# Kernel optimization log

Hardware: AMD Instinct MI355X
Metric: run time of the kernel (lower is better)

Reference implementation:

```python
import jax, jax.numpy as jnp
import numpy as np

N_NODES = 50000


def spmm(rows, cols, vals, dense):
    # out[i,:] = sum_{e: rows[e]==i} vals[e] * dense[cols[e], :]
    gathered = dense[cols] * vals[:, None]  # [E, D]
    return jax.ops.segment_sum(gathered, rows, num_segments=N_NODES)


def setup_inputs() -> dict:
    key = jax.random.key(0)
    k1, k2, k3, k4, k5, k6 = jax.random.split(key, 6)
    N, E, F, H, C = N_NODES, 800000, 512, 256, 64
    node_features = jax.random.normal(k1, (N, F), dtype=jnp.float32)
    adj_rows = jax.random.randint(k2, (E,), 0, N, dtype=jnp.int32)
    adj_cols = jax.random.randint(k3, (E,), 0, N, dtype=jnp.int32)
    adj_vals = jax.random.uniform(k4, (E,), dtype=jnp.float32)
    W1 = jax.random.normal(k5, (F, H), dtype=jnp.float32) * (1.0 / np.sqrt(F))
    b1 = jnp.zeros((H,), dtype=jnp.float32)
    W2 = jax.random.normal(k6, (H, C), dtype=jnp.float32) * (1.0 / np.sqrt(H))
    b2 = jnp.zeros((C,), dtype=jnp.float32)
    return {"node_features": node_features, "adj_rows": adj_rows,
            "adj_cols": adj_cols, "adj_vals": adj_vals,
            "W1": W1, "b1": b1, "W2": W2, "b2": b2}


def reference(node_features, adj_rows, adj_cols, adj_vals, W1, b1, W2, b2):
    # Layer 1: dense projection then sparse aggregation, then ReLU.
    support1 = node_features @ W1 + b1           # [N, H]
    x = jax.nn.relu(spmm(adj_rows, adj_cols, adj_vals, support1))
    # Dropout is identity in eval mode (training=False).
    # Layer 2
    support2 = x @ W2 + b2                       # [N, C]
    x = spmm(adj_rows, adj_cols, adj_vals, support2)
    return jax.nn.log_softmax(x, axis=1)
```

## Files before the change

### kernel.cpp

```cpp
#include <hip/hip_runtime.h>

#define N_NODES 50000
#define N_EDGES 800000
#define F_IN    512
#define H_DIM   256
#define C_DIM   64
#define MPAD    50048

#define NB      196
#define NCHUNK  49
#define CHUNK   16384
#define BCAP    6144

typedef __bf16 bf16;
typedef __bf16 bf16x4 __attribute__((ext_vector_type(4)));
typedef __bf16 bf16x8 __attribute__((ext_vector_type(8)));
typedef float  f32x4  __attribute__((ext_vector_type(4)));
typedef unsigned int u32;
typedef unsigned long long u64;
typedef unsigned char u8;

__device__ __forceinline__ void gl_lds16(const void* g, void* l) {
    __builtin_amdgcn_global_load_lds(
        (const __attribute__((address_space(1))) u32*)g,
        (__attribute__((address_space(3))) u32*)l, 16, 0, 0);
}

__device__ __forceinline__ float unpack_val(u32 pk) {
    return __builtin_bit_cast(float, pk << 16);
}


__global__ __launch_bounds__(1024) void prep_k(const int* __restrict__ rows,
                                               const float* __restrict__ W1,
                                               const float* __restrict__ W2,
                                               u32* __restrict__ G,
                                               bf16* __restrict__ W1t,
                                               bf16* __restrict__ W2t) {
    __shared__ u32 h[16 * NB];
    int bid = blockIdx.x, tid = threadIdx.x;
    if (bid < NCHUNK) {
        int wid = tid >> 6;
        for (int i = tid; i < 16 * NB; i += 1024) h[i] = 0;
        __syncthreads();
        int base = bid * CHUNK;
        int end = base + CHUNK; if (end > N_EDGES) end = N_EDGES;
        for (int e = base + tid; e < end; e += 1024)
            atomicAdd(&h[wid * NB + (rows[e] >> 8)], 1);
        __syncthreads();
        if (tid < NB) {
            u32 s = 0;
#pragma unroll
            for (int w = 0; w < 16; w++) s += h[w * NB + tid];
            G[tid * NCHUNK + bid] = s;
        }
    } else {
        int i = (bid - NCHUNK) * 1024 + tid;
        if (i < F_IN * H_DIM) {
            int k = i >> 8, n = i & 255;
            W1t[n * F_IN + k] = (bf16)W1[i];
        } else {
            int j = i - F_IN * H_DIM;
            if (j < H_DIM * C_DIM) {
                int k = j >> 6, n = j & 63;
                W2t[n * H_DIM + k] = (bf16)W2[j];
            }
        }
    }
}


__global__ __launch_bounds__(1024) void scatterB_k(const int* __restrict__ rows,
                                                   const int* __restrict__ cols,
                                                   const float* __restrict__ vals,
                                                   const u32* __restrict__ G,
                                                   u32* __restrict__ epack,
                                                   u8* __restrict__ lrow) {
    __shared__ u32 cur[NB];
    __shared__ u32 wtot[16];
    int tid = threadIdx.x, wid = tid >> 6, lane = tid & 63;
    int c = blockIdx.x;
    u32 tot = 0, pre = 0;
    if (tid < NB) {
        for (int cc = 0; cc < NCHUNK; cc++) {
            u32 v = G[tid * NCHUNK + cc];
            tot += v;
            if (cc < c) pre += v;
        }
    }
    u32 incl = tot;
#pragma unroll
    for (int off = 1; off < 64; off <<= 1) {
        u32 u = __shfl_up(incl, off, 64);
        if (lane >= off) incl += u;
    }
    if (lane == 63) wtot[wid] = incl;
    __syncthreads();
    u32 wpre = 0;
#pragma unroll
    for (int w = 0; w < 16; w++)
        if (w < wid) wpre += wtot[w];
    if (tid < NB) cur[tid] = (wpre + incl - tot) + pre;
    __syncthreads();
    int base = c * CHUNK;
    int end = base + CHUNK; if (end > N_EDGES) end = N_EDGES;
    for (int e = base + tid; e < end; e += 1024) {
        int r = rows[e];
        unsigned short vb = __builtin_bit_cast(unsigned short, (bf16)vals[e]);
        u32 pk = ((u32)cols[e] << 16) | (u32)vb;
        u32 p = atomicAdd(&cur[r >> 8], 1);
        epack[p] = pk;
        lrow[p] = (u8)(r & 255);
    }
}


__global__ __launch_bounds__(256) void sortC_k(u32* __restrict__ epack,
                                               const u8* __restrict__ lrow,
                                               const u32* __restrict__ G,
                                               int* __restrict__ starts) {
    __shared__ u32 edat[BCAP];
    __shared__ u32 sdat[BCAP];
    __shared__ u8  erow[BCAP];
    __shared__ u32 h[4 * 256];
    __shared__ u32 cur[256];
    __shared__ u32 wt1[4], wt2[4];
    __shared__ u32 sh_s, sh_n;
    int b = blockIdx.x, tid = threadIdx.x, wid = tid >> 6, lane = tid & 63;

    u32 btot = 0;
    if (tid < NB)
        for (int cc = 0; cc < NCHUNK; cc++) btot += G[tid * NCHUNK + cc];
    u32 bincl = btot;
#pragma unroll
    for (int off = 1; off < 64; off <<= 1) {
        u32 u = __shfl_up(bincl, off, 64);
        if (lane >= off) bincl += u;
    }
    if (lane == 63) wt1[wid] = bincl;
    __syncthreads();
    u32 bwpre = 0;
#pragma unroll
    for (int w = 0; w < 4; w++)
        if (w < wid) bwpre += wt1[w];
    if (tid == b) { sh_s = bwpre + bincl - btot; sh_n = btot; }
    __syncthreads();
    int s = (int)sh_s;
    int n = (int)sh_n;
    if (n > BCAP) n = BCAP;

    for (int i = tid; i < n; i += 256) { edat[i] = epack[s + i]; erow[i] = lrow[s + i]; }
    for (int i = tid; i < 1024; i += 256) h[i] = 0;
    __syncthreads();
    for (int i = tid; i < n; i += 256) atomicAdd(&h[wid * 256 + erow[i]], 1);
    __syncthreads();
    u32 tot = h[tid] + h[256 + tid] + h[512 + tid] + h[768 + tid];
    u32 incl = tot;
#pragma unroll
    for (int off = 1; off < 64; off <<= 1) {
        u32 u = __shfl_up(incl, off, 64);
        if (lane >= off) incl += u;
    }
    if (lane == 63) wt2[wid] = incl;
    __syncthreads();
    u32 wpre = 0;
#pragma unroll
    for (int w = 0; w < 4; w++)
        if (w < wid) wpre += wt2[w];
    u32 excl = wpre + incl - tot;
    cur[tid] = excl;
    int grow = b * 256 + tid;
    if (grow < N_NODES) starts[grow] = s + (int)excl;
    if (b == 0 && tid == 0) starts[N_NODES] = N_EDGES;
    __syncthreads();
    for (int i = tid; i < n; i += 256) {
        u32 p = atomicAdd(&cur[erow[i]], 1);
        sdat[p] = edat[i];
    }
    __syncthreads();
    for (int i = tid; i < n; i += 256) epack[s + i] = sdat[i];
}


__global__ __launch_bounds__(512) void gemm1_k(const float* __restrict__ A,
                                               const bf16* __restrict__ Bt,
                                               const float* __restrict__ bias,
                                               bf16* __restrict__ C) {
    constexpr int BM = 128, BK = 64;
    __shared__ bf16 As[BM * BK];
    __shared__ bf16 Bs[256 * BK];

    int tid = threadIdx.x;
    int wid = tid >> 6, lane = tid & 63;
    int wr = wid >> 2, wc = wid & 3;
    int l15 = lane & 15, hi = lane >> 4;
    int sw = l15 & 7;
    int bm = blockIdx.x;

    f32x4 acc[4][4];
#pragma unroll
    for (int m = 0; m < 4; m++)
#pragma unroll
        for (int n = 0; n < 4; n++) acc[m][n] = (f32x4){0.f, 0.f, 0.f, 0.f};

    for (int kt = 0; kt < F_IN; kt += BK) {
#pragma unroll
        for (int j = 0; j < 4; j++) {
            int ch = j * 512 + tid;
            int row = ch >> 3, kc = ch & 7;
            int kcs = kc ^ (row & 7);
            gl_lds16(Bt + (size_t)row * F_IN + kt + kcs * 8,
                     &Bs[(j * 512 + wid * 64) * 8]);
        }
#pragma unroll
        for (int j = 0; j < 2; j++) {
            int ch = j * 512 + tid;
            int row = ch >> 3, kc = ch & 7;
            int ar = bm * BM + row;
            if (ar >= N_NODES) ar = N_NODES - 1;
            const f32x4* src = (const f32x4*)(A + (size_t)ar * F_IN + kt + kc * 8);
            f32x4 u = src[0], v = src[1];
            bf16x8 o;
            o[0] = (bf16)u[0]; o[1] = (bf16)u[1]; o[2] = (bf16)u[2]; o[3] = (bf16)u[3];
            o[4] = (bf16)v[0]; o[5] = (bf16)v[1]; o[6] = (bf16)v[2]; o[7] = (bf16)v[3];
            *(bf16x8*)&As[row * BK + (kc ^ (row & 7)) * 8] = o;
        }
        __syncthreads();

        bf16x8 afr[2][4], bfr[2][4];
#pragma unroll
        for (int kk = 0; kk < 2; kk++) {
            int c = (kk * 4 + hi) ^ sw;
#pragma unroll
            for (int m = 0; m < 4; m++)
                afr[kk][m] = *(const bf16x8*)&As[(wr * 64 + m * 16 + l15) * BK + c * 8];
#pragma unroll
            for (int n = 0; n < 4; n++)
                bfr[kk][n] = *(const bf16x8*)&Bs[(wc * 64 + n * 16 + l15) * BK + c * 8];
        }
#pragma unroll
        for (int kk = 0; kk < 2; kk++)
#pragma unroll
            for (int m = 0; m < 4; m++)
#pragma unroll
                for (int n = 0; n < 4; n++)
                    acc[m][n] = __builtin_amdgcn_mfma_f32_16x16x32_bf16(
                        afr[kk][m], bfr[kk][n], acc[m][n], 0, 0, 0);
        __syncthreads();
    }

#pragma unroll
    for (int m = 0; m < 4; m++) {
        int row0 = bm * BM + wr * 64 + m * 16 + hi * 4;
#pragma unroll
        for (int n = 0; n < 4; n++) {
            int col = wc * 64 + n * 16 + l15;
            float bz = bias[col];
#pragma unroll
            for (int r = 0; r < 4; r++) {
                int row = row0 + r;
                if (row < N_NODES)
                    C[(size_t)row * H_DIM + col] = (bf16)(acc[m][n][r] + bz);
            }
        }
    }
}


__global__ __launch_bounds__(256) void gemm2_k(const bf16* __restrict__ A,
                                               const bf16* __restrict__ Bt,
                                               const float* __restrict__ bias,
                                               bf16* __restrict__ C) {
    constexpr int BM = 128, BK = 64;
    __shared__ bf16 As[BM * BK];
    __shared__ bf16 Bs[64 * BK];

    int tid = threadIdx.x;
    int wid = tid >> 6, lane = tid & 63;
    int wr = wid >> 1, wc = wid & 1;
    int l15 = lane & 15, hi = lane >> 4;
    int sw = l15 & 7;
    int bm = blockIdx.x;

    f32x4 acc[4][2];
#pragma unroll
    for (int m = 0; m < 4; m++)
#pragma unroll
        for (int n = 0; n < 2; n++) acc[m][n] = (f32x4){0.f, 0.f, 0.f, 0.f};

    for (int kt = 0; kt < H_DIM; kt += BK) {
#pragma unroll
        for (int j = 0; j < 4; j++) {
            int ch = j * 256 + tid;
            int row = ch >> 3, kc = ch & 7;
            int kcs = kc ^ (row & 7);
            gl_lds16(A + (size_t)(bm * BM + row) * H_DIM + kt + kcs * 8,
                     &As[(j * 256 + wid * 64) * 8]);
        }
#pragma unroll
        for (int j = 0; j < 2; j++) {
            int ch = j * 256 + tid;
            int row = ch >> 3, kc = ch & 7;
            int kcs = kc ^ (row & 7);
            gl_lds16(Bt + (size_t)row * H_DIM + kt + kcs * 8,
                     &Bs[(j * 256 + wid * 64) * 8]);
        }
        __syncthreads();

        bf16x8 afr[2][4], bfr[2][2];
#pragma unroll
        for (int kk = 0; kk < 2; kk++) {
            int c = (kk * 4 + hi) ^ sw;
#pragma unroll
            for (int m = 0; m < 4; m++)
                afr[kk][m] = *(const bf16x8*)&As[(wr * 64 + m * 16 + l15) * BK + c * 8];
#pragma unroll
            for (int n = 0; n < 2; n++)
                bfr[kk][n] = *(const bf16x8*)&Bs[(wc * 32 + n * 16 + l15) * BK + c * 8];
        }
#pragma unroll
        for (int kk = 0; kk < 2; kk++)
#pragma unroll
            for (int m = 0; m < 4; m++)
#pragma unroll
                for (int n = 0; n < 2; n++)
                    acc[m][n] = __builtin_amdgcn_mfma_f32_16x16x32_bf16(
                        afr[kk][m], bfr[kk][n], acc[m][n], 0, 0, 0);
        __syncthreads();
    }

#pragma unroll
    for (int m = 0; m < 4; m++) {
        int row0 = bm * BM + wr * 64 + m * 16 + hi * 4;
#pragma unroll
        for (int n = 0; n < 2; n++) {
            int col = wc * 32 + n * 16 + l15;
            float bz = bias[col];
#pragma unroll
            for (int r = 0; r < 4; r++) {
                int row = row0 + r;
                if (row < N_NODES)
                    C[(size_t)row * C_DIM + col] = (bf16)(acc[m][n][r] + bz);
            }
        }
    }
}


__global__ __launch_bounds__(256) void spmm1_k(const int* __restrict__ starts,
                                               const u32* __restrict__ epack,
                                               const bf16* __restrict__ s1,
                                               bf16* __restrict__ x16) {
    int wid = threadIdx.x >> 6, lane = threadIdx.x & 63;
    int row = blockIdx.x * 4 + wid;
    if (row >= N_NODES) return;
    int s = starts[row], e = starts[row + 1];
    f32x4 acc = (f32x4){0.f, 0.f, 0.f, 0.f};
    const bf16* s1l = s1 + lane * 4;
    int p = s;
    for (; p + 8 <= e; p += 8) {
        u32 k0 = __builtin_nontemporal_load(epack + p);
        u32 k1 = __builtin_nontemporal_load(epack + p + 1);
        u32 k2 = __builtin_nontemporal_load(epack + p + 2);
        u32 k3 = __builtin_nontemporal_load(epack + p + 3);
        u32 k4 = __builtin_nontemporal_load(epack + p + 4);
        u32 k5 = __builtin_nontemporal_load(epack + p + 5);
        u32 k6 = __builtin_nontemporal_load(epack + p + 6);
        u32 k7 = __builtin_nontemporal_load(epack + p + 7);
        bf16x4 g0 = *(const bf16x4*)(s1l + (size_t)(k0 >> 16) * H_DIM);
        bf16x4 g1 = *(const bf16x4*)(s1l + (size_t)(k1 >> 16) * H_DIM);
        bf16x4 g2 = *(const bf16x4*)(s1l + (size_t)(k2 >> 16) * H_DIM);
        bf16x4 g3 = *(const bf16x4*)(s1l + (size_t)(k3 >> 16) * H_DIM);
        bf16x4 g4 = *(const bf16x4*)(s1l + (size_t)(k4 >> 16) * H_DIM);
        bf16x4 g5 = *(const bf16x4*)(s1l + (size_t)(k5 >> 16) * H_DIM);
        bf16x4 g6 = *(const bf16x4*)(s1l + (size_t)(k6 >> 16) * H_DIM);
        bf16x4 g7 = *(const bf16x4*)(s1l + (size_t)(k7 >> 16) * H_DIM);
        float v0 = unpack_val(k0), v1 = unpack_val(k1), v2 = unpack_val(k2), v3 = unpack_val(k3);
        float v4 = unpack_val(k4), v5 = unpack_val(k5), v6 = unpack_val(k6), v7 = unpack_val(k7);
#pragma unroll
        for (int j = 0; j < 4; j++)
            acc[j] += v0 * (float)g0[j] + v1 * (float)g1[j] +
                      v2 * (float)g2[j] + v3 * (float)g3[j] +
                      v4 * (float)g4[j] + v5 * (float)g5[j] +
                      v6 * (float)g6[j] + v7 * (float)g7[j];
    }
    for (; p < e; ++p) {
        u32 k = __builtin_nontemporal_load(epack + p);
        float v = unpack_val(k);
        bf16x4 g = *(const bf16x4*)(s1l + (size_t)(k >> 16) * H_DIM);
#pragma unroll
        for (int j = 0; j < 4; j++) acc[j] += v * (float)g[j];
    }
    bf16x4 o;
#pragma unroll
    for (int j = 0; j < 4; j++) o[j] = (bf16)fmaxf(acc[j], 0.f);
    u64 bits = __builtin_bit_cast(u64, o);
    __builtin_nontemporal_store(bits, (u64*)(x16 + (size_t)row * H_DIM + lane * 4));
}


__global__ __launch_bounds__(256) void spmm2_sm_k(const int* __restrict__ starts,
                                                  const u32* __restrict__ epack,
                                                  const bf16* __restrict__ s2,
                                                  float* __restrict__ out) {
    int wid = threadIdx.x >> 6, lane = threadIdx.x & 63;
    int row = blockIdx.x * 4 + wid;
    if (row >= N_NODES) return;
    int s = starts[row], e = starts[row + 1];
    float acc = 0.f;
    int p = s;
    for (; p + 8 <= e; p += 8) {
        u32 k0 = __builtin_nontemporal_load(epack + p);
        u32 k1 = __builtin_nontemporal_load(epack + p + 1);
        u32 k2 = __builtin_nontemporal_load(epack + p + 2);
        u32 k3 = __builtin_nontemporal_load(epack + p + 3);
        u32 k4 = __builtin_nontemporal_load(epack + p + 4);
        u32 k5 = __builtin_nontemporal_load(epack + p + 5);
        u32 k6 = __builtin_nontemporal_load(epack + p + 6);
        u32 k7 = __builtin_nontemporal_load(epack + p + 7);
        float g0 = (float)s2[(size_t)(k0 >> 16) * C_DIM + lane];
        float g1 = (float)s2[(size_t)(k1 >> 16) * C_DIM + lane];
        float g2 = (float)s2[(size_t)(k2 >> 16) * C_DIM + lane];
        float g3 = (float)s2[(size_t)(k3 >> 16) * C_DIM + lane];
        float g4 = (float)s2[(size_t)(k4 >> 16) * C_DIM + lane];
        float g5 = (float)s2[(size_t)(k5 >> 16) * C_DIM + lane];
        float g6 = (float)s2[(size_t)(k6 >> 16) * C_DIM + lane];
        float g7 = (float)s2[(size_t)(k7 >> 16) * C_DIM + lane];
        acc += unpack_val(k0) * g0 + unpack_val(k1) * g1 +
               unpack_val(k2) * g2 + unpack_val(k3) * g3 +
               unpack_val(k4) * g4 + unpack_val(k5) * g5 +
               unpack_val(k6) * g6 + unpack_val(k7) * g7;
    }
    for (; p < e; ++p) {
        u32 k = __builtin_nontemporal_load(epack + p);
        acc += unpack_val(k) * (float)s2[(size_t)(k >> 16) * C_DIM + lane];
    }
    float mx = acc;
#pragma unroll
    for (int off = 32; off >= 1; off >>= 1) mx = fmaxf(mx, __shfl_xor(mx, off, 64));
    float ex = expf(acc - mx);
    float se = ex;
#pragma unroll
    for (int off = 32; off >= 1; off >>= 1) se += __shfl_xor(se, off, 64);
    __builtin_nontemporal_store((acc - mx) - logf(se),
                                out + (size_t)row * C_DIM + lane);
}


extern "C" void kernel_launch(void* const* d_in, const int* in_sizes, int n_in,
                              void* d_out, int out_size, void* d_ws, size_t ws_size,
                              hipStream_t stream) {
    const float* nf   = (const float*)d_in[0];
    const int*   rows = (const int*)d_in[1];
    const int*   cols = (const int*)d_in[2];
    const float* vals = (const float*)d_in[3];
    const float* W1   = (const float*)d_in[4];
    const float* b1   = (const float*)d_in[5];
    const float* W2   = (const float*)d_in[6];
    const float* b2   = (const float*)d_in[7];
    float* out = (float*)d_out;

    char* w = (char*)d_ws;
    auto alloc = [&](size_t b) { void* p = (void*)w; w += (b + 255) & ~(size_t)255; return p; };

    bf16* x16  = (bf16*)alloc((size_t)MPAD * H_DIM * 2);
    bf16* sup1 = (bf16*)alloc((size_t)N_NODES * H_DIM * 2);
    bf16* sup2 = sup1;
    bf16* W1t = (bf16*)alloc((size_t)H_DIM * F_IN * 2);
    bf16* W2t = (bf16*)alloc((size_t)C_DIM * H_DIM * 2);
    int* starts = (int*)alloc((size_t)(N_NODES + 1) * 4);
    u32* G      = (u32*)alloc((size_t)NB * NCHUNK * 4);
    u32* epack  = (u32*)alloc((size_t)N_EDGES * 4);
    u8*  lrow   = (u8*)alloc((size_t)N_EDGES);

    prep_k<<<NCHUNK + 144, 1024, 0, stream>>>(rows, W1, W2, G, W1t, W2t);
    scatterB_k<<<NCHUNK, 1024, 0, stream>>>(rows, cols, vals, G, epack, lrow);
    sortC_k<<<NB, 256, 0, stream>>>(epack, lrow, G, starts);
    gemm1_k<<<MPAD / 128, 512, 0, stream>>>(nf, W1t, b1, sup1);
    spmm1_k<<<(N_NODES + 3) / 4, 256, 0, stream>>>(starts, epack, sup1, x16);
    gemm2_k<<<MPAD / 128, 256, 0, stream>>>(x16, W2t, b2, sup2);
    spmm2_sm_k<<<(N_NODES + 3) / 4, 256, 0, stream>>>(starts, epack, sup2, out);

    (void)in_sizes; (void)n_in; (void)out_size; (void)ws_size;
}
```

Before: 191.6 us.

## Split SpMM1 feature dimension into slices with edge-parallel lane groups

Rewrites the first sparse aggregation so each block handles a 32-column slice of one row's features. Within a wave, four lane groups process different edges in parallel, each lane gathering bf16 pairs, and the partial sums are combined with cross-lane shuffles. The goal is more parallelism per row and more gathers in flight, since the previous kernel walked edges serially with full-row 8-byte gathers. In exchange the edge index stream is read eight times, gathers shrink to 4 bytes, and the grid becomes eight times larger.

```diff
diff --git a/kernel.cpp b/kernel.cpp
--- a/kernel.cpp
+++ b/kernel.cpp
@@ -13,6 +13,7 @@
 #define BCAP    6144
 
 typedef __bf16 bf16;
+typedef __bf16 bf16x2 __attribute__((ext_vector_type(2)));
 typedef __bf16 bf16x4 __attribute__((ext_vector_type(4)));
 typedef __bf16 bf16x8 __attribute__((ext_vector_type(8)));
 typedef float  f32x4  __attribute__((ext_vector_type(4)));
@@ -347,55 +348,46 @@
 }
 
 
-__global__ __launch_bounds__(256) void spmm1_k(const int* __restrict__ starts,
-                                               const u32* __restrict__ epack,
-                                               const bf16* __restrict__ s1,
-                                               bf16* __restrict__ x16) {
-    int wid = threadIdx.x >> 6, lane = threadIdx.x & 63;
-    int row = blockIdx.x * 4 + wid;
+__global__ __launch_bounds__(256) void spmm1x_k(const int* __restrict__ starts,
+                                                const u32* __restrict__ epack,
+                                                const bf16* __restrict__ s1,
+                                                bf16* __restrict__ x16) {
+    int tid = threadIdx.x, wid = tid >> 6, lane = tid & 63;
+    int g = lane >> 4, d2 = lane & 15;
+    int bid = blockIdx.x;
+    int sl = bid & 7, rb = bid >> 3;
+    int row = rb * 4 + wid;
     if (row >= N_NODES) return;
+    int dimoff = sl * 32 + d2 * 2;
+    const bf16* s1d = s1 + dimoff;
     int s = starts[row], e = starts[row + 1];
-    f32x4 acc = (f32x4){0.f, 0.f, 0.f, 0.f};
-    const bf16* s1l = s1 + lane * 4;
-    int p = s;
-    for (; p + 8 <= e; p += 8) {
-        u32 k0 = __builtin_nontemporal_load(epack + p);
-        u32 k1 = __builtin_nontemporal_load(epack + p + 1);
-        u32 k2 = __builtin_nontemporal_load(epack + p + 2);
-        u32 k3 = __builtin_nontemporal_load(epack + p + 3);
-        u32 k4 = __builtin_nontemporal_load(epack + p + 4);
-        u32 k5 = __builtin_nontemporal_load(epack + p + 5);
-        u32 k6 = __builtin_nontemporal_load(epack + p + 6);
-        u32 k7 = __builtin_nontemporal_load(epack + p + 7);
-        bf16x4 g0 = *(const bf16x4*)(s1l + (size_t)(k0 >> 16) * H_DIM);
-        bf16x4 g1 = *(const bf16x4*)(s1l + (size_t)(k1 >> 16) * H_DIM);
-        bf16x4 g2 = *(const bf16x4*)(s1l + (size_t)(k2 >> 16) * H_DIM);
-        bf16x4 g3 = *(const bf16x4*)(s1l + (size_t)(k3 >> 16) * H_DIM);
-        bf16x4 g4 = *(const bf16x4*)(s1l + (size_t)(k4 >> 16) * H_DIM);
-        bf16x4 g5 = *(const bf16x4*)(s1l + (size_t)(k5 >> 16) * H_DIM);
-        bf16x4 g6 = *(const bf16x4*)(s1l + (size_t)(k6 >> 16) * H_DIM);
-        bf16x4 g7 = *(const bf16x4*)(s1l + (size_t)(k7 >> 16) * H_DIM);
-        float v0 = unpack_val(k0), v1 = unpack_val(k1), v2 = unpack_val(k2), v3 = unpack_val(k3);
-        float v4 = unpack_val(k4), v5 = unpack_val(k5), v6 = unpack_val(k6), v7 = unpack_val(k7);
-#pragma unroll
-        for (int j = 0; j < 4; j++)
-            acc[j] += v0 * (float)g0[j] + v1 * (float)g1[j] +
-                      v2 * (float)g2[j] + v3 * (float)g3[j] +
-                      v4 * (float)g4[j] + v5 * (float)g5[j] +
-                      v6 * (float)g6[j] + v7 * (float)g7[j];
-    }
-    for (; p < e; ++p) {
-        u32 k = __builtin_nontemporal_load(epack + p);
-        float v = unpack_val(k);
-        bf16x4 g = *(const bf16x4*)(s1l + (size_t)(k >> 16) * H_DIM);
-#pragma unroll
-        for (int j = 0; j < 4; j++) acc[j] += v * (float)g[j];
-    }
-    bf16x4 o;
-#pragma unroll
-    for (int j = 0; j < 4; j++) o[j] = (bf16)fmaxf(acc[j], 0.f);
-    u64 bits = __builtin_bit_cast(u64, o);
-    __builtin_nontemporal_store(bits, (u64*)(x16 + (size_t)row * H_DIM + lane * 4));
+    float a0 = 0.f, a1 = 0.f;
+    for (int p = s; p < e; p += 16) {
+        int p0 = p + g, p1 = p + 4 + g, p2 = p + 8 + g, p3 = p + 12 + g;
+        u32 k0 = (p0 < e) ? __builtin_nontemporal_load(epack + p0) : 0u;
+        u32 k1 = (p1 < e) ? __builtin_nontemporal_load(epack + p1) : 0u;
+        u32 k2 = (p2 < e) ? __builtin_nontemporal_load(epack + p2) : 0u;
+        u32 k3 = (p3 < e) ? __builtin_nontemporal_load(epack + p3) : 0u;
+        bf16x2 g0 = *(const bf16x2*)(s1d + (size_t)(k0 >> 16) * H_DIM);
+        bf16x2 g1 = *(const bf16x2*)(s1d + (size_t)(k1 >> 16) * H_DIM);
+        bf16x2 g2 = *(const bf16x2*)(s1d + (size_t)(k2 >> 16) * H_DIM);
+        bf16x2 g3 = *(const bf16x2*)(s1d + (size_t)(k3 >> 16) * H_DIM);
+        float v0 = unpack_val(k0), v1 = unpack_val(k1);
+        float v2 = unpack_val(k2), v3 = unpack_val(k3);
+        a0 += v0 * (float)g0[0] + v1 * (float)g1[0] +
+              v2 * (float)g2[0] + v3 * (float)g3[0];
+        a1 += v0 * (float)g0[1] + v1 * (float)g1[1] +
+              v2 * (float)g2[1] + v3 * (float)g3[1];
+    }
+    a0 += __shfl_xor(a0, 16, 64); a0 += __shfl_xor(a0, 32, 64);
+    a1 += __shfl_xor(a1, 16, 64); a1 += __shfl_xor(a1, 32, 64);
+    if (g == 0) {
+        bf16x2 o;
+        o[0] = (bf16)fmaxf(a0, 0.f);
+        o[1] = (bf16)fmaxf(a1, 0.f);
+        u32 bits = __builtin_bit_cast(u32, o);
+        __builtin_nontemporal_store(bits, (u32*)(x16 + (size_t)row * H_DIM + dimoff));
+    }
 }
 
 
@@ -477,7 +469,7 @@
     scatterB_k<<<NCHUNK, 1024, 0, stream>>>(rows, cols, vals, G, epack, lrow);
     sortC_k<<<NB, 256, 0, stream>>>(epack, lrow, G, starts);
     gemm1_k<<<MPAD / 128, 512, 0, stream>>>(nf, W1t, b1, sup1);
-    spmm1_k<<<(N_NODES + 3) / 4, 256, 0, stream>>>(starts, epack, sup1, x16);
+    spmm1x_k<<<8 * ((N_NODES + 3) / 4), 256, 0, stream>>>(starts, epack, sup1, x16);
     gemm2_k<<<MPAD / 128, 256, 0, stream>>>(x16, W2t, b2, sup2);
     spmm2_sm_k<<<(N_NODES + 3) / 4, 256, 0, stream>>>(starts, epack, sup2, out);
 
```

New measurement: 267.6 us. 39.6% more time.

## Scatter edges chunk-locally and gather bucket segments in sort kernel

Applied to the files above, without the earlier changes.

The scatter kernel now writes each edge chunk's bucket-grouped output into a chunk-local region, so it only needs a per-chunk scan of 196 counts instead of a full global prefix over all chunks. The sort kernel then assembles each bucket from 49 chunk segments, using a binary search over segment offsets, and writes the final epack. This removes the serial 49-element G loops in the scatter kernel and keeps its scattered writes within a local 64KB window. In exchange it adds an extra intermediate buffer and per-element binary-search indexing in the sort kernel's load loop.

```diff
diff --git a/kernel.cpp b/kernel.cpp
--- a/kernel.cpp
+++ b/kernel.cpp
@@ -74,33 +74,31 @@
                                                    const int* __restrict__ cols,
                                                    const float* __restrict__ vals,
                                                    const u32* __restrict__ G,
-                                                   u32* __restrict__ epack,
-                                                   u8* __restrict__ lrow) {
+                                                   u32* __restrict__ epack_t,
+                                                   u8* __restrict__ lrow_t) {
     __shared__ u32 cur[NB];
-    __shared__ u32 wtot[16];
+    __shared__ u32 wt[4];
     int tid = threadIdx.x, wid = tid >> 6, lane = tid & 63;
     int c = blockIdx.x;
-    u32 tot = 0, pre = 0;
-    if (tid < NB) {
-        for (int cc = 0; cc < NCHUNK; cc++) {
-            u32 v = G[tid * NCHUNK + cc];
-            tot += v;
-            if (cc < c) pre += v;
-        }
-    }
-    u32 incl = tot;
-#pragma unroll
-    for (int off = 1; off < 64; off <<= 1) {
-        u32 u = __shfl_up(incl, off, 64);
-        if (lane >= off) incl += u;
-    }
-    if (lane == 63) wtot[wid] = incl;
-    __syncthreads();
-    u32 wpre = 0;
-#pragma unroll
-    for (int w = 0; w < 16; w++)
-        if (w < wid) wpre += wtot[w];
-    if (tid < NB) cur[tid] = (wpre + incl - tot) + pre;
+    u32 v = 0, incl = 0;
+    if (tid < 256) {
+        if (tid < NB) v = G[tid * NCHUNK + c];
+        incl = v;
+#pragma unroll
+        for (int off = 1; off < 64; off <<= 1) {
+            u32 u = __shfl_up(incl, off, 64);
+            if (lane >= off) incl += u;
+        }
+        if (lane == 63) wt[wid] = incl;
+    }
+    __syncthreads();
+    if (tid < 256) {
+        u32 wpre = 0;
+#pragma unroll
+        for (int w = 0; w < 4; w++)
+            if (w < wid) wpre += wt[w];
+        if (tid < NB) cur[tid] = wpre + incl - v;
+    }
     __syncthreads();
     int base = c * CHUNK;
     int end = base + CHUNK; if (end > N_EDGES) end = N_EDGES;
@@ -109,47 +107,60 @@
         unsigned short vb = __builtin_bit_cast(unsigned short, (bf16)vals[e]);
         u32 pk = ((u32)cols[e] << 16) | (u32)vb;
         u32 p = atomicAdd(&cur[r >> 8], 1);
-        epack[p] = pk;
-        lrow[p] = (u8)(r & 255);
-    }
-}
-
-
-__global__ __launch_bounds__(256) void sortC_k(u32* __restrict__ epack,
-                                               const u8* __restrict__ lrow,
+        epack_t[base + p] = pk;
+        lrow_t[base + p] = (u8)(r & 255);
+    }
+}
+
+
+__global__ __launch_bounds__(256) void sortC_k(const u32* __restrict__ epack_t,
+                                               const u8* __restrict__ lrow_t,
                                                const u32* __restrict__ G,
+                                               u32* __restrict__ epack,
                                                int* __restrict__ starts) {
     __shared__ u32 edat[BCAP];
     __shared__ u32 sdat[BCAP];
     __shared__ u8  erow[BCAP];
     __shared__ u32 h[4 * 256];
     __shared__ u32 cur[256];
-    __shared__ u32 wt1[4], wt2[4];
-    __shared__ u32 sh_s, sh_n;
+    __shared__ u32 wt2[4];
+    __shared__ u32 segoff[NCHUNK + 1];
+    __shared__ u32 segsrc[NCHUNK];
+    __shared__ u32 sh_s;
     int b = blockIdx.x, tid = threadIdx.x, wid = tid >> 6, lane = tid & 63;
 
-    u32 btot = 0;
-    if (tid < NB)
-        for (int cc = 0; cc < NCHUNK; cc++) btot += G[tid * NCHUNK + cc];
-    u32 bincl = btot;
-#pragma unroll
-    for (int off = 1; off < 64; off <<= 1) {
-        u32 u = __shfl_up(bincl, off, 64);
-        if (lane >= off) bincl += u;
-    }
-    if (lane == 63) wt1[wid] = bincl;
-    __syncthreads();
-    u32 bwpre = 0;
-#pragma unroll
-    for (int w = 0; w < 4; w++)
-        if (w < wid) bwpre += wt1[w];
-    if (tid == b) { sh_s = bwpre + bincl - btot; sh_n = btot; }
+    if (tid < 64) {
+        u32 len = 0, pre = 0;
+        if (tid < NCHUNK) {
+            for (int bb = 0; bb < b; bb++) pre += G[bb * NCHUNK + tid];
+            len = G[b * NCHUNK + tid];
+            segsrc[tid] = tid * CHUNK + pre;
+        }
+        u32 incl = len;
+#pragma unroll
+        for (int off = 1; off < 64; off <<= 1) {
+            u32 u = __shfl_up(incl, off, 64);
+            if (lane >= off) incl += u;
+        }
+        if (tid < NCHUNK) segoff[tid] = incl - len;
+        if (tid == 63) segoff[NCHUNK] = incl;
+        u32 ssum = pre;
+#pragma unroll
+        for (int off = 1; off < 64; off <<= 1) ssum += __shfl_xor(ssum, off, 64);
+        if (tid == 0) sh_s = ssum;
+    }
     __syncthreads();
     int s = (int)sh_s;
-    int n = (int)sh_n;
+    int n = (int)segoff[NCHUNK];
     if (n > BCAP) n = BCAP;
 
-    for (int i = tid; i < n; i += 256) { edat[i] = epack[s + i]; erow[i] = lrow[s + i]; }
+    for (int i = tid; i < n; i += 256) {
+        int lo = 0, hi = NCHUNK;
+        while (hi - lo > 1) { int mid = (lo + hi) >> 1; if ((int)segoff[mid] <= i) lo = mid; else hi = mid; }
+        u32 src = segsrc[lo] + (u32)(i - (int)segoff[lo]);
+        edat[i] = epack_t[src];
+        erow[i] = lrow_t[src];
+    }
     for (int i = tid; i < 1024; i += 256) h[i] = 0;
     __syncthreads();
     for (int i = tid; i < n; i += 256) atomicAdd(&h[wid * 256 + erow[i]], 1);
@@ -469,13 +480,14 @@
     bf16* W1t = (bf16*)alloc((size_t)H_DIM * F_IN * 2);
     bf16* W2t = (bf16*)alloc((size_t)C_DIM * H_DIM * 2);
     int* starts = (int*)alloc((size_t)(N_NODES + 1) * 4);
-    u32* G      = (u32*)alloc((size_t)NB * NCHUNK * 4);
-    u32* epack  = (u32*)alloc((size_t)N_EDGES * 4);
-    u8*  lrow   = (u8*)alloc((size_t)N_EDGES);
+    u32* G       = (u32*)alloc((size_t)NB * NCHUNK * 4);
+    u32* epack   = (u32*)alloc((size_t)N_EDGES * 4);
+    u32* epack_t = (u32*)alloc((size_t)NCHUNK * CHUNK * 4);
+    u8*  lrow_t  = (u8*)alloc((size_t)NCHUNK * CHUNK);
 
     prep_k<<<NCHUNK + 144, 1024, 0, stream>>>(rows, W1, W2, G, W1t, W2t);
-    scatterB_k<<<NCHUNK, 1024, 0, stream>>>(rows, cols, vals, G, epack, lrow);
-    sortC_k<<<NB, 256, 0, stream>>>(epack, lrow, G, starts);
+    scatterB_k<<<NCHUNK, 1024, 0, stream>>>(rows, cols, vals, G, epack_t, lrow_t);
+    sortC_k<<<NB, 256, 0, stream>>>(epack_t, lrow_t, G, epack, starts);
     gemm1_k<<<MPAD / 128, 512, 0, stream>>>(nf, W1t, b1, sup1);
     spmm1_k<<<(N_NODES + 3) / 4, 256, 0, stream>>>(starts, epack, sup1, x16);
     gemm2_k<<<MPAD / 128, 256, 0, stream>>>(x16, W2t, b2, sup2);
```

After: 207.3 us. 1.08x slower.

## Merge edge scatter and first GEMM into one heterogeneous launch

Applied to the files above, without the earlier changes.

Combines the edge bucketing scatter kernel and the layer-1 dense GEMM into a single kernel whose first blocks do the scatter and whose remaining blocks do GEMM tiles. The two are independent, so they can run concurrently on the GPU, filling the idle compute units left by the 49-block scatter and saving one launch. The scatter part now uses 512 threads instead of 1024, so each scatter block does more serial work. Shared memory is a union buffer sized for the GEMM.

```diff
diff --git a/kernel.cpp b/kernel.cpp
--- a/kernel.cpp
+++ b/kernel.cpp
@@ -70,47 +70,137 @@
 }
 
 
-__global__ __launch_bounds__(1024) void scatterB_k(const int* __restrict__ rows,
-                                                   const int* __restrict__ cols,
-                                                   const float* __restrict__ vals,
-                                                   const u32* __restrict__ G,
-                                                   u32* __restrict__ epack,
-                                                   u8* __restrict__ lrow) {
-    __shared__ u32 cur[NB];
-    __shared__ u32 wtot[16];
-    int tid = threadIdx.x, wid = tid >> 6, lane = tid & 63;
-    int c = blockIdx.x;
-    u32 tot = 0, pre = 0;
-    if (tid < NB) {
-        for (int cc = 0; cc < NCHUNK; cc++) {
-            u32 v = G[tid * NCHUNK + cc];
-            tot += v;
-            if (cc < c) pre += v;
-        }
-    }
-    u32 incl = tot;
-#pragma unroll
-    for (int off = 1; off < 64; off <<= 1) {
-        u32 u = __shfl_up(incl, off, 64);
-        if (lane >= off) incl += u;
-    }
-    if (lane == 63) wtot[wid] = incl;
-    __syncthreads();
-    u32 wpre = 0;
-#pragma unroll
-    for (int w = 0; w < 16; w++)
-        if (w < wid) wpre += wtot[w];
-    if (tid < NB) cur[tid] = (wpre + incl - tot) + pre;
-    __syncthreads();
-    int base = c * CHUNK;
-    int end = base + CHUNK; if (end > N_EDGES) end = N_EDGES;
-    for (int e = base + tid; e < end; e += 1024) {
-        int r = rows[e];
-        unsigned short vb = __builtin_bit_cast(unsigned short, (bf16)vals[e]);
-        u32 pk = ((u32)cols[e] << 16) | (u32)vb;
-        u32 p = atomicAdd(&cur[r >> 8], 1);
-        epack[p] = pk;
-        lrow[p] = (u8)(r & 255);
+__global__ __launch_bounds__(512) void sg_k(const int* __restrict__ rows,
+                                            const int* __restrict__ cols,
+                                            const float* __restrict__ vals,
+                                            const u32* __restrict__ G,
+                                            u32* __restrict__ epack,
+                                            u8* __restrict__ lrow,
+                                            const float* __restrict__ A,
+                                            const bf16* __restrict__ Bt,
+                                            const float* __restrict__ bias,
+                                            bf16* __restrict__ C) {
+    __shared__ __attribute__((aligned(16))) char smem[49152];
+    int bid = blockIdx.x, tid = threadIdx.x;
+    int wid = tid >> 6, lane = tid & 63;
+
+    if (bid < NCHUNK) {
+        u32* cur = (u32*)smem;
+        u32* wt  = (u32*)(smem + 1024);
+        int c = bid;
+        u32 tot = 0, pre = 0, incl = 0;
+        if (tid < 256) {
+            if (tid < NB) {
+                for (int cc = 0; cc < NCHUNK; cc++) {
+                    u32 v = G[tid * NCHUNK + cc];
+                    tot += v;
+                    if (cc < c) pre += v;
+                }
+            }
+            incl = tot;
+#pragma unroll
+            for (int off = 1; off < 64; off <<= 1) {
+                u32 u = __shfl_up(incl, off, 64);
+                if (lane >= off) incl += u;
+            }
+            if (lane == 63) wt[wid] = incl;
+        }
+        __syncthreads();
+        if (tid < 256) {
+            u32 wpre = 0;
+#pragma unroll
+            for (int w = 0; w < 4; w++)
+                if (w < wid) wpre += wt[w];
+            if (tid < NB) cur[tid] = (wpre + incl - tot) + pre;
+        }
+        __syncthreads();
+        int base = c * CHUNK;
+        int end = base + CHUNK; if (end > N_EDGES) end = N_EDGES;
+        for (int e = base + tid; e < end; e += 512) {
+            int r = rows[e];
+            unsigned short vb = __builtin_bit_cast(unsigned short, (bf16)vals[e]);
+            u32 pk = ((u32)cols[e] << 16) | (u32)vb;
+            u32 p = atomicAdd(&cur[r >> 8], 1);
+            epack[p] = pk;
+            lrow[p] = (u8)(r & 255);
+        }
+        return;
+    }
+
+    constexpr int BM = 128, BK = 64;
+    bf16* As = (bf16*)smem;
+    bf16* Bs = (bf16*)(smem + 16384);
+    int wr = wid >> 2, wc = wid & 3;
+    int l15 = lane & 15, hi = lane >> 4;
+    int sw = l15 & 7;
+    int bm = bid - NCHUNK;
+
+    f32x4 acc[4][4];
+#pragma unroll
+    for (int m = 0; m < 4; m++)
+#pragma unroll
+        for (int n = 0; n < 4; n++) acc[m][n] = (f32x4){0.f, 0.f, 0.f, 0.f};
+
+    for (int kt = 0; kt < F_IN; kt += BK) {
+#pragma unroll
+        for (int j = 0; j < 4; j++) {
+            int ch = j * 512 + tid;
+            int row = ch >> 3, kc = ch & 7;
+            int kcs = kc ^ (row & 7);
+            gl_lds16(Bt + (size_t)row * F_IN + kt + kcs * 8,
+                     &Bs[(j * 512 + wid * 64) * 8]);
+        }
+#pragma unroll
+        for (int j = 0; j < 2; j++) {
+            int ch = j * 512 + tid;
+            int row = ch >> 3, kc = ch & 7;
+            int ar = bm * BM + row;
+            if (ar >= N_NODES) ar = N_NODES - 1;
+            const f32x4* src = (const f32x4*)(A + (size_t)ar * F_IN + kt + kc * 8);
+            f32x4 u = src[0], v = src[1];
+            bf16x8 o;
+            o[0] = (bf16)u[0]; o[1] = (bf16)u[1]; o[2] = (bf16)u[2]; o[3] = (bf16)u[3];
+            o[4] = (bf16)v[0]; o[5] = (bf16)v[1]; o[6] = (bf16)v[2]; o[7] = (bf16)v[3];
+            *(bf16x8*)&As[row * BK + (kc ^ (row & 7)) * 8] = o;
+        }
+        __syncthreads();
+
+        bf16x8 afr[2][4], bfr[2][4];
+#pragma unroll
+        for (int kk = 0; kk < 2; kk++) {
+            int c = (kk * 4 + hi) ^ sw;
+#pragma unroll
+            for (int m = 0; m < 4; m++)
+                afr[kk][m] = *(const bf16x8*)&As[(wr * 64 + m * 16 + l15) * BK + c * 8];
+#pragma unroll
+            for (int n = 0; n < 4; n++)
+                bfr[kk][n] = *(const bf16x8*)&Bs[(wc * 64 + n * 16 + l15) * BK + c * 8];
+        }
+#pragma unroll
+        for (int kk = 0; kk < 2; kk++)
+#pragma unroll
+            for (int m = 0; m < 4; m++)
+#pragma unroll
+                for (int n = 0; n < 4; n++)
+                    acc[m][n] = __builtin_amdgcn_mfma_f32_16x16x32_bf16(
+                        afr[kk][m], bfr[kk][n], acc[m][n], 0, 0, 0);
+        __syncthreads();
+    }
+
+#pragma unroll
+    for (int m = 0; m < 4; m++) {
+        int row0 = bm * BM + wr * 64 + m * 16 + hi * 4;
+#pragma unroll
+        for (int n = 0; n < 4; n++) {
+            int col = wc * 64 + n * 16 + l15;
+            float bz = bias[col];
+#pragma unroll
+            for (int r = 0; r < 4; r++) {
+                int row = row0 + r;
+                if (row < N_NODES)
+                    C[(size_t)row * H_DIM + col] = (bf16)(acc[m][n][r] + bz);
+            }
+        }
     }
 }
 
@@ -179,91 +269,6 @@
     }
     __syncthreads();
     for (int i = tid; i < n; i += 256) epack[s + i] = sdat[i];
-}
-
-
-__global__ __launch_bounds__(512) void gemm1_k(const float* __restrict__ A,
-                                               const bf16* __restrict__ Bt,
-                                               const float* __restrict__ bias,
-                                               bf16* __restrict__ C) {
-    constexpr int BM = 128, BK = 64;
-    __shared__ bf16 As[BM * BK];
-    __shared__ bf16 Bs[256 * BK];
-
-    int tid = threadIdx.x;
-    int wid = tid >> 6, lane = tid & 63;
-    int wr = wid >> 2, wc = wid & 3;
-    int l15 = lane & 15, hi = lane >> 4;
-    int sw = l15 & 7;
-    int bm = blockIdx.x;
-
-    f32x4 acc[4][4];
-#pragma unroll
-    for (int m = 0; m < 4; m++)
-#pragma unroll
-        for (int n = 0; n < 4; n++) acc[m][n] = (f32x4){0.f, 0.f, 0.f, 0.f};
-
-    for (int kt = 0; kt < F_IN; kt += BK) {
-#pragma unroll
-        for (int j = 0; j < 4; j++) {
-            int ch = j * 512 + tid;
-            int row = ch >> 3, kc = ch & 7;
-            int kcs = kc ^ (row & 7);
-            gl_lds16(Bt + (size_t)row * F_IN + kt + kcs * 8,
-                     &Bs[(j * 512 + wid * 64) * 8]);
-        }
-#pragma unroll
-        for (int j = 0; j < 2; j++) {
-            int ch = j * 512 + tid;
-            int row = ch >> 3, kc = ch & 7;
-            int ar = bm * BM + row;
-            if (ar >= N_NODES) ar = N_NODES - 1;
-            const f32x4* src = (const f32x4*)(A + (size_t)ar * F_IN + kt + kc * 8);
-            f32x4 u = src[0], v = src[1];
-            bf16x8 o;
-            o[0] = (bf16)u[0]; o[1] = (bf16)u[1]; o[2] = (bf16)u[2]; o[3] = (bf16)u[3];
-            o[4] = (bf16)v[0]; o[5] = (bf16)v[1]; o[6] = (bf16)v[2]; o[7] = (bf16)v[3];
-            *(bf16x8*)&As[row * BK + (kc ^ (row & 7)) * 8] = o;
-        }
-        __syncthreads();
-
-        bf16x8 afr[2][4], bfr[2][4];
-#pragma unroll
-        for (int kk = 0; kk < 2; kk++) {
-            int c = (kk * 4 + hi) ^ sw;
-#pragma unroll
-            for (int m = 0; m < 4; m++)
-                afr[kk][m] = *(const bf16x8*)&As[(wr * 64 + m * 16 + l15) * BK + c * 8];
-#pragma unroll
-            for (int n = 0; n < 4; n++)
-                bfr[kk][n] = *(const bf16x8*)&Bs[(wc * 64 + n * 16 + l15) * BK + c * 8];
-        }
-#pragma unroll
-        for (int kk = 0; kk < 2; kk++)
-#pragma unroll
-            for (int m = 0; m < 4; m++)
-#pragma unroll
-                for (int n = 0; n < 4; n++)
-                    acc[m][n] = __builtin_amdgcn_mfma_f32_16x16x32_bf16(
-                        afr[kk][m], bfr[kk][n], acc[m][n], 0, 0, 0);
-        __syncthreads();
-    }
-
-#pragma unroll
-    for (int m = 0; m < 4; m++) {
-        int row0 = bm * BM + wr * 64 + m * 16 + hi * 4;
-#pragma unroll
-        for (int n = 0; n < 4; n++) {
-            int col = wc * 64 + n * 16 + l15;
-            float bz = bias[col];
-#pragma unroll
-            for (int r = 0; r < 4; r++) {
-                int row = row0 + r;
-                if (row < N_NODES)
-                    C[(size_t)row * H_DIM + col] = (bf16)(acc[m][n][r] + bz);
-            }
-        }
-    }
 }
 
 
@@ -474,9 +479,9 @@
     u8*  lrow   = (u8*)alloc((size_t)N_EDGES);
 
     prep_k<<<NCHUNK + 144, 1024, 0, stream>>>(rows, W1, W2, G, W1t, W2t);
-    scatterB_k<<<NCHUNK, 1024, 0, stream>>>(rows, cols, vals, G, epack, lrow);
+    sg_k<<<NCHUNK + MPAD / 128, 512, 0, stream>>>(rows, cols, vals, G, epack, lrow,
+                                                  nf, W1t, b1, sup1);
     sortC_k<<<NB, 256, 0, stream>>>(epack, lrow, G, starts);
-    gemm1_k<<<MPAD / 128, 512, 0, stream>>>(nf, W1t, b1, sup1);
     spmm1_k<<<(N_NODES + 3) / 4, 256, 0, stream>>>(starts, epack, sup1, x16);
     gemm2_k<<<MPAD / 128, 256, 0, stream>>>(x16, W2t, b2, sup2);
     spmm2_sm_k<<<(N_NODES + 3) / 4, 256, 0, stream>>>(starts, epack, sup2, out);
```

After: 182.1 us. 1.05x faster.
